# Kernel optimization log

Measured on AMD Instinct MI355X. Metric: run time of the kernel, lower is better.

## Reference

```python
import jax, jax.numpy as jnp
import numpy as np
from jax import lax

WIN = (9, 9, 9)
EPS = 1e-05


def _sum1d(x, axis, win):
    """Sliding-window sum of size `win` along `axis`, zero-padded (SAME)."""
    pad = win // 2
    pads = [(pad, pad) if a == axis else (0, 0) for a in range(x.ndim)]
    xp = jnp.pad(x, pads)
    c = jnp.cumsum(xp, axis=axis)
    c = jnp.pad(c, [(1, 0) if a == axis else (0, 0) for a in range(x.ndim)])
    n = x.shape[axis]
    return (lax.slice_in_dim(c, win, win + n, axis=axis)
            - lax.slice_in_dim(c, 0, n, axis=axis))


def _box_sum(x):
    """Separable 3D box-filter sum == conv3d with ones([9,9,9]), SAME pad."""
    for axis, w in zip((2, 3, 4), WIN):
        x = _sum1d(x, axis, w)
    return x


def setup_inputs() -> dict:
    key = jax.random.key(0)
    k1, k2 = jax.random.split(key)
    shape = (2, 1, 128, 128, 128)
    y_pred = jax.random.normal(k1, shape, dtype=jnp.float32)
    y_true = jax.random.normal(k2, shape, dtype=jnp.float32)
    return {"y_pred": y_pred, "y_true": y_true}


def reference(y_pred, y_true):
    I = y_true.astype(jnp.float32)
    J = y_pred.astype(jnp.float32)
    win_size = float(np.prod(WIN))  # 729

    I_sum = _box_sum(I)
    J_sum = _box_sum(J)
    I2_sum = _box_sum(I * I)
    J2_sum = _box_sum(J * J)
    IJ_sum = _box_sum(I * J)

    u_I = I_sum / win_size
    u_J = J_sum / win_size

    cross = IJ_sum - u_J * I_sum - u_I * J_sum + u_I * u_J * win_size
    I_var = I2_sum - 2 * u_I * I_sum + u_I * u_I * win_size
    J_var = J2_sum - 2 * u_J * J_sum + u_J * u_J * win_size

    cc_map = cross * cross / (I_var * J_var + EPS)
    return jnp.mean(-cc_map)
```

## Files before the change

kernel.cpp:

```cpp
#include <hip/hip_runtime.h>

#define DSZ 128
#define TX 16
#define TY 16
#define PY 24
#define NVOX 4194304.0f

__global__ void ncc_zero(float* out) { out[0] = 0.0f; }

__global__ __launch_bounds__(256) void ncc_main(const float* __restrict__ Iin,
                                                const float* __restrict__ Jin,
                                                float* __restrict__ out)
{
    const int tx0 = blockIdx.x * TX;
    const int ty0 = blockIdx.y * TY;
    const int b   = blockIdx.z >> 3;
    const int tz0 = (blockIdx.z & 7) * 16;
    const int tid = threadIdx.x;
    const int lx  = tid & 15;
    const int ly  = tid >> 4;

    const float* __restrict__ Ib = Iin + b * (DSZ * DSZ * DSZ);
    const float* __restrict__ Jb = Jin + b * (DSZ * DSZ * DSZ);

    __shared__ float2 sIJ[2][PY][26];
    __shared__ float4 s4m[2][PY][17];
    __shared__ float  s1m[2][PY][17];

    float rb0[9], rb1[9], rb2[9], rb3[9], rb4[9];
#pragma unroll
    for (int i = 0; i < 9; ++i) { rb0[i]=0.f; rb1[i]=0.f; rb2[i]=0.f; rb3[i]=0.f; rb4[i]=0.f; }
    float zs0=0.f, zs1=0.f, zs2=0.f, zs3=0.f, zs4=0.f;
    float acc = 0.f;

    for (int rnd = 0; rnd < 12; ++rnd) {
#pragma unroll
        for (int p = 0; p < 2; ++p) {
            const int zp = tz0 + 2 * rnd + p - 4;
            const bool zvalid = ((unsigned)zp < (unsigned)DSZ);
            for (int it = tid; it < PY * 12; it += 256) {
                const int r = it / 12;
                const int c = it - r * 12;
                const int gy = ty0 + r - 4;
                const int gx = tx0 + 2 * c - 4;
                float4 w = make_float4(0.f, 0.f, 0.f, 0.f);
                if (zvalid && (unsigned)gy < (unsigned)DSZ && (unsigned)gx < (unsigned)(DSZ - 1)) {
                    const int idx = (zp * DSZ + gy) * DSZ + gx;
                    const float2 vi = *(const float2*)(Ib + idx);
                    const float2 vj = *(const float2*)(Jb + idx);
                    w = make_float4(vi.x, vj.x, vi.y, vj.y);
                }
                *(float4*)&sIJ[p][r][2 * c] = w;
            }
        }
        __syncthreads();

        for (int it = tid; it < PY * TX; it += 256) {
            const int r = it >> 4;
            const int x = it & 15;
#pragma unroll
            for (int p = 0; p < 2; ++p) {
                float a = 0.f, bq = 0.f, aa = 0.f, bb = 0.f, ab = 0.f;
#pragma unroll
                for (int dx = 0; dx < 9; ++dx) {
                    const float2 v = sIJ[p][r][x + dx];
                    a += v.x; bq += v.y;
                    aa = fmaf(v.x, v.x, aa);
                    bb = fmaf(v.y, v.y, bb);
                    ab = fmaf(v.x, v.y, ab);
                }
                s4m[p][r][x] = make_float4(a, bq, aa, bb);
                s1m[p][r][x] = ab;
            }
        }
        __syncthreads();

#pragma unroll
        for (int p = 0; p < 2; ++p) {
            float y0 = 0.f, y1 = 0.f, y2 = 0.f, y3 = 0.f, y4 = 0.f;
#pragma unroll
            for (int dy = 0; dy < 9; ++dy) {
                const float4 t = s4m[p][ly + dy][lx];
                y0 += t.x; y1 += t.y; y2 += t.z; y3 += t.w;
                y4 += s1m[p][ly + dy][lx];
            }

            zs0 += y0 - rb0[0]; zs1 += y1 - rb1[0]; zs2 += y2 - rb2[0];
            zs3 += y3 - rb3[0]; zs4 += y4 - rb4[0];
#pragma unroll
            for (int i = 0; i < 8; ++i) {
                rb0[i]=rb0[i+1]; rb1[i]=rb1[i+1]; rb2[i]=rb2[i+1];
                rb3[i]=rb3[i+1]; rb4[i]=rb4[i+1];
            }
            rb0[8]=y0; rb1[8]=y1; rb2[8]=y2; rb3[8]=y3; rb4[8]=y4;

            const int zi = 2 * rnd + p;
            if (zi >= 8) {
                const float inv = 1.0f / 729.0f;
                const float uI = zs0 * inv;
                const float uJ = zs1 * inv;
                const float cross = zs4 - uJ * zs0 - uI * zs1 + uI * uJ * 729.0f;
                const float Ivar  = zs2 - 2.0f * uI * zs0 + uI * uI * 729.0f;
                const float Jvar  = zs3 - 2.0f * uJ * zs1 + uJ * uJ * 729.0f;
                acc += cross * cross / (Ivar * Jvar + 1e-5f);
            }
        }
    }

#pragma unroll
    for (int off = 32; off > 0; off >>= 1) acc += __shfl_down(acc, off);
    __shared__ float wpart[4];
    if ((tid & 63) == 0) wpart[tid >> 6] = acc;
    __syncthreads();
    if (tid == 0) {
        const float s = wpart[0] + wpart[1] + wpart[2] + wpart[3];
        atomicAdd(out, s * (-1.0f / NVOX));
    }
}

extern "C" void kernel_launch(void* const* d_in, const int* in_sizes, int n_in,
                              void* d_out, int out_size, void* d_ws, size_t ws_size,
                              hipStream_t stream)
{
    const float* J = (const float*)d_in[0];
    const float* I = (const float*)d_in[1];
    float* out = (float*)d_out;

    ncc_zero<<<dim3(1), dim3(1), 0, stream>>>(out);
    dim3 grid(DSZ / TX, DSZ / TY, 2 * (DSZ / 16));
    ncc_main<<<grid, dim3(256), 0, stream>>>(I, J, out);
}
```

Baseline: 61.78 us.

## Fuse global load with x-direction box sums via float4 loads and sliding window

Removes the staging shared buffer for raw I/J values. 192 threads each load three float4 chunks of I and J directly from global memory and compute four consecutive x-window sums in registers using a running add/subtract. The intermediate buffers are double-buffered by round parity, which removes one __syncthreads per round. The risk is that the sliding update changes floating-point rounding, and only 192 of 256 threads do the load/x-pass work, with more registers per thread.

```diff
diff --git a/kernel.cpp b/kernel.cpp
--- a/kernel.cpp
+++ b/kernel.cpp
@@ -23,9 +23,8 @@
     const float* __restrict__ Ib = Iin + b * (DSZ * DSZ * DSZ);
     const float* __restrict__ Jb = Jin + b * (DSZ * DSZ * DSZ);
 
-    __shared__ float2 sIJ[2][PY][26];
-    __shared__ float4 s4m[2][PY][17];
-    __shared__ float  s1m[2][PY][17];
+    __shared__ float4 s4m[4][PY][17];
+    __shared__ float4 s1v[4][PY][5];
 
     float rb0[9], rb1[9], rb2[9], rb3[9], rb4[9];
 #pragma unroll
@@ -34,55 +33,75 @@
     float acc = 0.f;
 
     for (int rnd = 0; rnd < 12; ++rnd) {
+        if (tid < 192) {
+            const int p   = (tid >= 96);
+            const int t2  = tid - p * 96;
+            const int r   = t2 >> 2;
+            const int xg  = t2 & 3;
+            const int zp  = tz0 + 2 * rnd + p - 4;
+            const int gy  = ty0 + r - 4;
+            const int gxb = tx0 + 4 * xg - 4;
+            const bool rowok = ((unsigned)zp < (unsigned)DSZ) &&
+                               ((unsigned)gy < (unsigned)DSZ);
+            const int zoff = (zp * DSZ + gy) * DSZ;
+
+            float vi[12], vj[12];
 #pragma unroll
-        for (int p = 0; p < 2; ++p) {
-            const int zp = tz0 + 2 * rnd + p - 4;
-            const bool zvalid = ((unsigned)zp < (unsigned)DSZ);
-            for (int it = tid; it < PY * 12; it += 256) {
-                const int r = it / 12;
-                const int c = it - r * 12;
-                const int gy = ty0 + r - 4;
-                const int gx = tx0 + 2 * c - 4;
-                float4 w = make_float4(0.f, 0.f, 0.f, 0.f);
-                if (zvalid && (unsigned)gy < (unsigned)DSZ && (unsigned)gx < (unsigned)(DSZ - 1)) {
-                    const int idx = (zp * DSZ + gy) * DSZ + gx;
-                    const float2 vi = *(const float2*)(Ib + idx);
-                    const float2 vj = *(const float2*)(Jb + idx);
-                    w = make_float4(vi.x, vj.x, vi.y, vj.y);
+            for (int g = 0; g < 3; ++g) {
+                const int gx = gxb + 4 * g;
+                float4 va = make_float4(0.f, 0.f, 0.f, 0.f);
+                float4 vb = va;
+                if (rowok && (unsigned)gx < (unsigned)DSZ) {
+                    va = *(const float4*)(Ib + zoff + gx);
+                    vb = *(const float4*)(Jb + zoff + gx);
                 }
-                *(float4*)&sIJ[p][r][2 * c] = w;
+                vi[4*g+0]=va.x; vi[4*g+1]=va.y; vi[4*g+2]=va.z; vi[4*g+3]=va.w;
+                vj[4*g+0]=vb.x; vj[4*g+1]=vb.y; vj[4*g+2]=vb.z; vj[4*g+3]=vb.w;
             }
-        }
-        __syncthreads();
 
-        for (int it = tid; it < PY * TX; it += 256) {
-            const int r = it >> 4;
-            const int x = it & 15;
+            float wI=0.f, wJ=0.f, wII=0.f, wJJ=0.f, wIJ=0.f;
 #pragma unroll
-            for (int p = 0; p < 2; ++p) {
-                float a = 0.f, bq = 0.f, aa = 0.f, bb = 0.f, ab = 0.f;
+            for (int k = 3; k < 9; ++k) {
+                wI += vi[k]; wJ += vj[k];
+                wII = fmaf(vi[k], vi[k], wII);
+                wJJ = fmaf(vj[k], vj[k], wJJ);
+                wIJ = fmaf(vi[k], vj[k], wIJ);
+            }
 #pragma unroll
-                for (int dx = 0; dx < 9; ++dx) {
-                    const float2 v = sIJ[p][r][x + dx];
-                    a += v.x; bq += v.y;
-                    aa = fmaf(v.x, v.x, aa);
-                    bb = fmaf(v.y, v.y, bb);
-                    ab = fmaf(v.x, v.y, ab);
-                }
-                s4m[p][r][x] = make_float4(a, bq, aa, bb);
-                s1m[p][r][x] = ab;
+            for (int k = 0; k < 3; ++k) {
+                wI += vi[k]; wJ += vj[k];
+                wII = fmaf(vi[k], vi[k], wII);
+                wJJ = fmaf(vj[k], vj[k], wJJ);
+                wIJ = fmaf(vi[k], vj[k], wIJ);
             }
+            const int sl = (rnd & 1) * 2 + p;
+            float mIJ[4];
+            s4m[sl][r][4*xg] = make_float4(wI, wJ, wII, wJJ);
+            mIJ[0] = wIJ;
+#pragma unroll
+            for (int j = 1; j < 4; ++j) {
+                const float ai = vi[8+j], aj = vj[8+j];
+                const float di = vi[j-1], dj = vj[j-1];
+                wI += ai - di; wJ += aj - dj;
+                wII += fmaf(ai, ai, -di * di);
+                wJJ += fmaf(aj, aj, -dj * dj);
+                wIJ += fmaf(ai, aj, -di * dj);
+                s4m[sl][r][4*xg + j] = make_float4(wI, wJ, wII, wJJ);
+                mIJ[j] = wIJ;
+            }
+            s1v[sl][r][xg] = make_float4(mIJ[0], mIJ[1], mIJ[2], mIJ[3]);
         }
         __syncthreads();
 
 #pragma unroll
         for (int p = 0; p < 2; ++p) {
-            float y0 = 0.f, y1 = 0.f, y2 = 0.f, y3 = 0.f, y4 = 0.f;
+            const int sl = (rnd & 1) * 2 + p;
+            float y0=0.f, y1=0.f, y2=0.f, y3=0.f, y4=0.f;
 #pragma unroll
             for (int dy = 0; dy < 9; ++dy) {
-                const float4 t = s4m[p][ly + dy][lx];
+                const float4 t = s4m[sl][ly + dy][lx];
                 y0 += t.x; y1 += t.y; y2 += t.z; y3 += t.w;
-                y4 += s1m[p][ly + dy][lx];
+                y4 += ((const float*)&s1v[sl][ly + dy][0])[lx];
             }
 
             zs0 += y0 - rb0[0]; zs1 += y1 - rb1[0]; zs2 += y2 - rb2[0];
```

New measurement: 49.80 us. 19.4% less time.
